# Performance work log

Measured on AMD Instinct MI355X. Metric: run time of the kernel, lower is better.

The kernel has to match this reference:

```python
import math
import jax, jax.numpy as jnp
import numpy as np
from jax.scipy.special import erf

D = 128                # cubic box / image size (even)
B, T = 4, 2            # particles, candidate poses per particle
GRID_DIST_DEGS = 8.0
GRID_STEP_DEGS = 2.0
PIXEL_SIZE = 1.5       # Angstrom / px
MAX_SHIFT_FRACTION = 0.2
TOP_K = 2
HALF_PARTICLE = 0.5 * D


def _rot_z(a):
    c, s = jnp.cos(a), jnp.sin(a)
    z, o = jnp.zeros_like(a), jnp.ones_like(a)
    return jnp.stack([jnp.stack([c, -s, z], -1),
                      jnp.stack([s, c, z], -1),
                      jnp.stack([z, z, o], -1)], -2)


def _rot_y(a):
    c, s = jnp.cos(a), jnp.sin(a)
    z, o = jnp.zeros_like(a), jnp.ones_like(a)
    return jnp.stack([jnp.stack([c, z, s], -1),
                      jnp.stack([z, o, z], -1),
                      jnp.stack([-s, z, c], -1)], -2)


def _euler_zyz_to_matrix(ang):
    # RELION convention ZYZ: R = Rz(a) @ Ry(b) @ Rz(c)
    return _rot_z(ang[..., 0]) @ _rot_y(ang[..., 1]) @ _rot_z(ang[..., 2])


def _so3_grid_rotmats():
    n = math.ceil(GRID_DIST_DEGS / GRID_STEP_DEGS)
    n = n if n % 2 == 1 else n + 1
    half = GRID_DIST_DEGS / 2.0
    a = np.linspace(-half, half, n)
    g = np.stack(np.meshgrid(a, a, a, indexing='ij'), -1).reshape(-1, 3)
    return _euler_zyz_to_matrix(jnp.deg2rad(jnp.asarray(g, jnp.float32)))


def _compute_dft(vol):
    # sinc^2 gridding pre-filter, then fftshifted rfftn of fftshifted volume
    d = vol.shape[-1]
    f = jnp.fft.fftshift(jnp.fft.fftfreq(d)).astype(vol.dtype)
    fz, fy, fx = jnp.meshgrid(f, f, f, indexing='ij')
    r = jnp.sqrt(fz * fz + fy * fy + fx * fx)
    vol = vol * jnp.sinc(r) ** 2
    dft = jnp.fft.rfftn(jnp.fft.fftshift(vol, axes=(-3, -2, -1)), axes=(-3, -2, -1))
    return jnp.fft.fftshift(dft, axes=(-3, -2))


def _trilinear_complex(vol, z, y, x):
    # trilinear interpolation into a complex 3D array, zero outside bounds
    Dz, Dy, Dx = vol.shape
    z0f, y0f, x0f = jnp.floor(z), jnp.floor(y), jnp.floor(x)
    fz, fy, fx = z - z0f, y - y0f, x - x0f
    z0, y0, x0 = z0f.astype(jnp.int32), y0f.astype(jnp.int32), x0f.astype(jnp.int32)

    def corner(zi, yi, xi, w):
        valid = (zi >= 0) & (zi < Dz) & (yi >= 0) & (yi < Dy) & (xi >= 0) & (xi < Dx)
        v = vol[jnp.clip(zi, 0, Dz - 1), jnp.clip(yi, 0, Dy - 1), jnp.clip(xi, 0, Dx - 1)]
        return jnp.where(valid, v * w, jnp.zeros((), vol.dtype))

    out = corner(z0, y0, x0, (1 - fz) * (1 - fy) * (1 - fx))
    out = out + corner(z0, y0, x0 + 1, (1 - fz) * (1 - fy) * fx)
    out = out + corner(z0, y0 + 1, x0, (1 - fz) * fy * (1 - fx))
    out = out + corner(z0, y0 + 1, x0 + 1, (1 - fz) * fy * fx)
    out = out + corner(z0 + 1, y0, x0, fz * (1 - fy) * (1 - fx))
    out = out + corner(z0 + 1, y0, x0 + 1, fz * (1 - fy) * fx)
    out = out + corner(z0 + 1, y0 + 1, x0, fz * fy * (1 - fx))
    out = out + corner(z0 + 1, y0 + 1, x0 + 1, fz * fy * fx)
    return out


def _extract_central_slices_rfft_3d(vol_rfft, d, rotmats):
    # rotated central-slice extraction from a fftshifted rfft 3D volume
    fy = jnp.fft.fftshift(jnp.fft.fftfreq(d)).astype(jnp.float32)
    fx = jnp.fft.rfftfreq(d).astype(jnp.float32)
    gy, gx = jnp.meshgrid(fy, fx, indexing='ij')            # (H, Wr)
    coords = jnp.stack([jnp.zeros_like(gy), gy, gx], -1)    # zyx, z=0 plane
    Rzyx = rotmats[..., ::-1, ::-1]                         # xyz rotmat -> zyx
    rot = jnp.einsum('...ij,hwj->...hwi', Rzyx, coords)     # (...,H,Wr,3)
    conj_mask = rot[..., 2] < 0                             # redundant half
    rot = jnp.where(conj_mask[..., None], -rot, rot)
    zi = rot[..., 0] * d + d // 2
    yi = rot[..., 1] * d + d // 2
    xi = rot[..., 2] * d
    s = _trilinear_complex(vol_rfft, zi, yi, xi)
    return jnp.where(conj_mask, jnp.conj(s), s)


def _forward(vol, imgs, ctf, rotmats, grid_rotmats):
    d = vol.shape[-1]
    vol_rfft = _compute_dft(vol)                            # (d, d, d//2+1)
    # _real_to_fourier
    fimg = jnp.fft.fftshift(
        jnp.fft.rfftn(jnp.fft.fftshift(imgs, axes=(-2, -1)), axes=(-2, -1)),
        axes=(-2,))                                         # (B, d, d//2+1)
    # compose pose candidates with the local SO3 grid: rotmats @ grid_rotmats
    exp_R = jnp.einsum('gjk,btij->btgik', grid_rotmats, rotmats)   # (B,T,G,3,3)
    projs = _extract_central_slices_rfft_3d(vol_rfft, d, exp_R)    # (B,T,G,H,Wr)
    projs = projs * ctf[:, None, None]
    # correlate_dft_2d
    prod = fimg[:, None, None] * jnp.conj(projs)
    prod = jnp.fft.ifftshift(prod, axes=(-2,))
    corrs = jnp.fft.ifftshift(jnp.fft.irfftn(prod, s=(d, d), axes=(-2, -1)),
                              axes=(-2, -1))                # (B,T,G,d,d) real
    # constrained peak search within max_shift_fraction window
    delta = math.ceil(d * (1.0 - MAX_SHIFT_FRACTION) / 2)
    h0 = delta
    c = corrs[..., h0:d - delta, h0:d - delta]
    maxJ = jnp.max(c, -1)
    argJ = jnp.argmax(c, -1)
    perImgCorr = jnp.max(maxJ, -1)                          # (B,T,G)
    argI = jnp.argmax(maxJ, -1)
    col = jnp.take_along_axis(argJ, argI[..., None], -1)[..., 0]
    shiftsXY = jnp.stack([h0 + col, h0 + argI], -1)         # (B,T,G,2) as (x,y)
    b = perImgCorr.shape[0]
    nrots = perImgCorr.shape[2]
    flat = perImgCorr.reshape(b, -1)                        # (B, T*G)
    maxCorrs, maxIdxs = jax.lax.top_k(flat, TOP_K)
    bestShifts = jnp.take_along_axis(shiftsXY.reshape(b, -1, 2),
                                     maxIdxs[..., None], axis=1)   # (B,K,2)
    mean = jnp.mean(flat, -1, keepdims=True)
    std = jnp.std(flat, -1, keepdims=True, ddof=1)
    comparedWeight = 0.5 * (1.0 + erf((maxCorrs - mean) / (std * 1.4142135623730951)))
    predShiftsAngs = -(bestShifts.astype(jnp.float32) - HALF_PARTICLE) * PIXEL_SIZE
    predRotMats = grid_rotmats[maxIdxs % nrots]             # (B,K,3,3)
    return maxCorrs, predRotMats, predShiftsAngs, comparedWeight


def setup_inputs() -> dict:
    key = jax.random.key(0)
    kv, ki, kc, kr = jax.random.split(key, 4)
    vol = jax.random.normal(kv, (D, D, D), jnp.float32)
    imgs = jax.random.normal(ki, (B, D, D), jnp.float32)
    ctf = jax.random.uniform(kc, (B, D, D // 2 + 1), jnp.float32, -1.0, 1.0)
    ang = jax.random.uniform(kr, (B, T, 3), jnp.float32, -np.pi, np.pi)
    rotmats = _euler_zyz_to_matrix(ang)
    grid_rotmats = _so3_grid_rotmats()
    return {"vol": vol, "imgs": imgs, "ctf": ctf, "rotmats": rotmats,
            "grid_rotmats": grid_rotmats}


def reference(vol, imgs, ctf, rotmats, grid_rotmats):
    return _forward(vol, imgs, ctf, rotmats, grid_rotmats)
```

## Files before the change

### kernel.cpp

```cpp
#include <hip/hip_runtime.h>
#include <hip/hip_fp16.h>
#include <math.h>
#include <float.h>

#define DD   128
#define KX   65
#define NB   4
#define NTT  2
#define NG   125
#define NBTG (NB*NTT*NG)
#define WIN  24
#define H0   52

#define QZ  132
#define QY  131
#define QX  68
#define QPLANE (QY*QX)
#define QN  (QZ*QY*QX)

typedef unsigned int u32;

__device__ __forceinline__ float2 cmul(float2 a, float2 b){
    return make_float2(a.x*b.x - a.y*b.y, a.x*b.y + a.y*b.x);
}

__device__ __forceinline__ void make_tw(float2* sTw, int tid){
    if (tid < 128){
        float s, c;
        sincosf((float)tid * (float)(M_PI/64.0), &s, &c);
        sTw[tid] = make_float2(c, s);
    }
}

__global__ __launch_bounds__(256) void k_stageA(const float* __restrict__ vol,
                       const float* __restrict__ imgs,
                       float2* __restrict__ A1, float2* __restrict__ B1,
                       uint4* __restrict__ Yz, int n4){
    __shared__ float2 sZ [16*DD];
    __shared__ float2 sZ2[16*DD];
    __shared__ float2 sTw[128];
    __shared__ float  sSinc[257];
    int tid = threadIdx.x;
    int bid = blockIdx.x;

    if (bid >= 642){
        int i = (bid - 642)*256 + tid;
        for (; i < n4; i += 256*256)
            Yz[i] = make_uint4(0,0,0,0);
        return;
    }
    make_tw(sTw, tid);

    if (bid < 512){
        for (int i = tid; i < 257; i += 256){
            float t = (float)i * (0.75f/256.f);
            float r = sqrtf(t);
            float s = (r > 0.f) ? (sinf((float)M_PI*r)/((float)M_PI*r)) : 1.f;
            sSinc[i] = s*s;
        }
        __syncthreads();
        int z = bid >> 2, q = bid & 3;
        int y0 = q*32;
        float fz = (z-64)*(1.0f/128.0f);
        float fz2 = fz*fz;
        for (int i = tid; i < 16*DD; i += 256){
            int p = i >> 7, x = i & 127;
            int yA = y0 + 2*p;
            float fx = (x-64)*(1.0f/128.0f);
            float fyA = (yA-64)*(1.0f/128.0f);
            float fyB = fyA + (1.0f/128.0f);
            float b2 = fz2 + fx*fx;
            float tA = (b2 + fyA*fyA) * (256.f/0.75f);
            float tB = (b2 + fyB*fyB) * (256.f/0.75f);
            int iA = min((int)tA, 255), iB = min((int)tB, 255);
            float frA = tA - (float)iA, frB = tB - (float)iB;
            float wA = sSinc[iA] + frA*(sSinc[iA+1]-sSinc[iA]);
            float wB = sSinc[iB] + frB*(sSinc[iB+1]-sSinc[iB]);
            float a = vol[(z*DD + yA)*DD + x] * wA;
            float b = vol[(z*DD + yA+1)*DD + x] * wB;
            sZ[i] = make_float2(a, b);
        }
        __syncthreads();
        for (int i = tid; i < 16*32; i += 256){
            int p = i >> 5, x1 = i & 31;
            int b0 = p*DD + x1;
            float2 a = sZ[b0], bb = sZ[b0+32], c2 = sZ[b0+64], d = sZ[b0+96];
            float acx=a.x+c2.x, acy=a.y+c2.y;
            float amx=a.x-c2.x, amy=a.y-c2.y;
            float bdx=bb.x+d.x, bdy=bb.y+d.y;
            float bmx=bb.x-d.x, bmy=bb.y-d.y;
            sZ[b0   ] = make_float2(acx+bdx, acy+bdy);
            sZ[b0+32] = make_float2(amx+bmy, amy-bmx);
            sZ[b0+64] = make_float2(acx-bdx, acy-bdy);
            sZ[b0+96] = make_float2(amx-bmy, amy+bmx);
        }
        __syncthreads();
        for (int i = tid; i < 16*32; i += 256){
            int p = i >> 5, r5 = i & 31;
            int c = r5 >> 3, x2 = r5 & 7;
            int b0 = p*DD + 32*c + x2;
            float2 u0 = sZ[b0], u1 = sZ[b0+8], u2 = sZ[b0+16], u3 = sZ[b0+24];
            float2 w1 = sTw[(8*c)&127];  w1.y = -w1.y;
            float2 w2 = sTw[(16*c)&127]; w2.y = -w2.y;
            float2 w3 = sTw[(24*c)&127]; w3.y = -w3.y;
            float2 t1 = cmul(u1,w1), t2 = cmul(u2,w2), t3 = cmul(u3,w3);
            float2 pp = make_float2(u0.x+t2.x, u0.y+t2.y);
            float2 qq = make_float2(u0.x-t2.x, u0.y-t2.y);
            float2 rr = make_float2(t1.x+t3.x, t1.y+t3.y);
            float2 ss = make_float2(t1.x-t3.x, t1.y-t3.y);
            sZ[b0   ] = make_float2(pp.x+rr.x, pp.y+rr.y);
            sZ[b0+8 ] = make_float2(qq.x+ss.y, qq.y-ss.x);
            sZ[b0+16] = make_float2(pp.x-rr.x, pp.y-rr.y);
            sZ[b0+24] = make_float2(qq.x-ss.y, qq.y+ss.x);
        }
        __syncthreads();
        for (int i = tid; i < 16*DD; i += 256){
            int p = i >> 7, k = i & 127;
            int c = k & 3, s = (k >> 2) & 3;
            const float2* v = &sZ[p*DD + 32*c + 8*s];
            float ar0=0,ai0=0,ar1=0,ai1=0;
            int j = 0;
            #pragma unroll
            for (int x2 = 0; x2 < 8; x2 += 2){
                float2 v0 = v[x2], v1 = v[x2+1];
                float2 e0 = sTw[j]; int jn = (j + k)&127;
                float2 e1 = sTw[jn];
                ar0 += v0.x*e0.x + v0.y*e0.y;  ai0 += v0.y*e0.x - v0.x*e0.y;
                ar1 += v1.x*e1.x + v1.y*e1.y;  ai1 += v1.y*e1.x - v1.x*e1.y;
                j = (jn + k)&127;
            }
            sZ2[i] = make_float2(ar0+ar1, ai0+ai1);
        }
        __syncthreads();
        for (int i = tid; i < 16*KX; i += 256){
            int p = i / KX, k = i - p*KX;
            float2 Zk = sZ2[p*DD + k];
            float2 Zm = sZ2[p*DD + ((128-k)&127)];
            float2 A = make_float2(0.5f*(Zk.x+Zm.x), 0.5f*(Zk.y-Zm.y));
            float Dx = Zk.x - Zm.x, Dy = Zk.y + Zm.y;
            float2 Bv = make_float2(0.5f*Dy, -0.5f*Dx);
            int yA = y0 + 2*p;
            A1[(z*DD + yA  )*KX + k] = A;
            A1[(z*DD + yA+1)*KX + k] = Bv;
        }
    } else {
        __syncthreads();
        int o = (bid - 512)*256 + tid;
        if (o >= NB*DD*KX) return;
        int b = o / (DD*KX);
        int r = o - b*DD*KX;
        int y = r / KX, k = r - y*KX;
        const float* row = imgs + (b*DD + y)*DD;
        float ar0=0,ai0=0,ar1=0,ai1=0,ar2=0,ai2=0,ar3=0,ai3=0;
        int i0=0, i1=k&127, i2=(2*k)&127, i3=(3*k)&127;
        int st = (4*k)&127;
        for (int x = 0; x < DD; x += 4){
            float v0=row[x], v1=row[x+1], v2=row[x+2], v3=row[x+3];
            float2 e0=sTw[i0], e1=sTw[i1], e2=sTw[i2], e3=sTw[i3];
            ar0 += v0*e0.x; ai0 -= v0*e0.y;
            ar1 += v1*e1.x; ai1 -= v1*e1.y;
            ar2 += v2*e2.x; ai2 -= v2*e2.y;
            ar3 += v3*e3.x; ai3 -= v3*e3.y;
            i0=(i0+st)&127; i1=(i1+st)&127; i2=(i2+st)&127; i3=(i3+st)&127;
        }
        B1[o] = make_float2(ar0+ar1+ar2+ar3, ai0+ai1+ai2+ai3);
    }
}

__global__ __launch_bounds__(256) void k_stageB(const float2* __restrict__ A1,
                       const float* __restrict__ ctf, const float2* __restrict__ B1,
                       float2* __restrict__ A2, float2* __restrict__ Fc){
    __shared__ float2 sU[32*KX];
    __shared__ float2 sTw[128];
    int tid = threadIdx.x;
    int bid = blockIdx.x;
    make_tw(sTw, tid);
    __syncthreads();

    if (bid < 512){
        int z = bid >> 2, c = bid & 3;
        const float2* base = A1 + z*DD*KX;
        for (int i = tid; i < 32*KX; i += 256){
            int n = i / KX, kk = i - n*KX;
            float2 a  = base[(n    )*KX + kk];
            float2 bb = base[(n+32)*KX + kk];
            float2 c2 = base[(n+64)*KX + kk];
            float2 d  = base[(n+96)*KX + kk];
            float acx = a.x + c2.x, acy = a.y + c2.y;
            float amx = a.x - c2.x, amy = a.y - c2.y;
            float bdx = bb.x + d.x, bdy = bb.y + d.y;
            float bmx = bb.x - d.x, bmy = bb.y - d.y;
            float2 u;
            if (c == 0)      u = make_float2(acx + bdx, acy + bdy);
            else if (c == 2) u = make_float2(acx - bdx, acy - bdy);
            else if (c == 1) u = make_float2(amx + bmy, amy - bmx);
            else             u = make_float2(amx - bmy, amy + bmx);
            sU[i] = u;
        }
        __syncthreads();
        float2 w1 = sTw[(8*c)&127];  w1.y = -w1.y;
        float2 w2 = sTw[(16*c)&127]; w2.y = -w2.y;
        float2 w3 = sTw[(24*c)&127]; w3.y = -w3.y;
        for (int i = tid; i < 8*KX; i += 256){
            int n2 = i / KX, kk = i - n2*KX;
            int b0 = n2*KX + kk;
            float2 u0 = sU[b0], u1 = sU[b0+8*KX], u2 = sU[b0+16*KX], u3 = sU[b0+24*KX];
            float2 t1 = cmul(u1,w1), t2 = cmul(u2,w2), t3 = cmul(u3,w3);
            float2 p = make_float2(u0.x+t2.x, u0.y+t2.y);
            float2 q = make_float2(u0.x-t2.x, u0.y-t2.y);
            float2 r = make_float2(t1.x+t3.x, t1.y+t3.y);
            float2 s = make_float2(t1.x-t3.x, t1.y-t3.y);
            sU[b0       ] = make_float2(p.x+r.x, p.y+r.y);
            sU[b0+ 8*KX ] = make_float2(q.x+s.y, q.y-s.x);
            sU[b0+16*KX ] = make_float2(p.x-r.x, p.y-r.y);
            sU[b0+24*KX ] = make_float2(q.x-s.y, q.y+s.x);
        }
        __syncthreads();
        for (int o = tid; o < 32*KX; o += 256){
            int m = o / KX, kk = o - m*KX;
            int ky = 4*m + c;
            int s4 = m & 3;
            const float2* v = &sU[(8*s4)*KX + kk];
            float ar0=0,ai0=0,ar1=0,ai1=0;
            int j = 0;
            #pragma unroll
            for (int n2 = 0; n2 < 8; n2 += 2){
                float2 v0 = v[n2*KX], v1 = v[(n2+1)*KX];
                float2 e0 = sTw[j]; int jn = (j + ky)&127;
                float2 e1 = sTw[jn];
                ar0 += v0.x*e0.x + v0.y*e0.y;  ai0 += v0.y*e0.x - v0.x*e0.y;
                ar1 += v1.x*e1.x + v1.y*e1.y;  ai1 += v1.y*e1.x - v1.x*e1.y;
                j = (jn + ky)&127;
            }
            A2[(z*DD + ky)*KX + kk] = make_float2(ar0+ar1, ai0+ai1);
        }
    } else {
        int o = (bid - 512)*256 + tid;
        if (o >= NB*DD*KX) return;
        int b = o / (DD*KX);
        int r = o - b*DD*KX;
        int h = r / KX, k = r - h*KX;
        int kky = (h + 64) & 127;
        const float2* col = B1 + b*DD*KX + k;
        float ar0=0,ai0=0,ar1=0,ai1=0,ar2=0,ai2=0,ar3=0,ai3=0;
        int i0=0, i1=kky&127, i2=(2*kky)&127, i3=(3*kky)&127;
        int st = (4*kky)&127;
        for (int y = 0; y < DD; y += 4){
            float2 v0=col[(y+0)*KX], v1=col[(y+1)*KX];
            float2 v2=col[(y+2)*KX], v3=col[(y+3)*KX];
            float2 e0=sTw[i0], e1=sTw[i1], e2=sTw[i2], e3=sTw[i3];
            ar0 += v0.x*e0.x + v0.y*e0.y;  ai0 += v0.y*e0.x - v0.x*e0.y;
            ar1 += v1.x*e1.x + v1.y*e1.y;  ai1 += v1.y*e1.x - v1.x*e1.y;
            ar2 += v2.x*e2.x + v2.y*e2.y;  ai2 += v2.y*e2.x - v2.x*e2.y;
            ar3 += v3.x*e3.x + v3.y*e3.y;  ai3 += v3.y*e3.x - v3.x*e3.y;
            i0=(i0+st)&127; i1=(i1+st)&127; i2=(i2+st)&127; i3=(i3+st)&127;
        }
        float sgn = ((h + k)&1) ? -1.f : 1.f;
        float cf = ctf[o];
        Fc[o] = make_float2((ar0+ar1+ar2+ar3)*sgn*cf, (ai0+ai1+ai2+ai3)*sgn*cf);
    }
}

__global__ __launch_bounds__(256) void k_volD(const float2* __restrict__ A2,
                       u32* __restrict__ Yh){
    __shared__ float2 sU[32*KX];
    __shared__ float2 sTw[128];
    int tid = threadIdx.x;
    int bid = blockIdx.x;
    int ky = bid >> 2, c = bid & 3;
    make_tw(sTw, tid);
    __syncthreads();

    const float2* base = A2 + ky*KX;
    for (int i = tid; i < 32*KX; i += 256){
        int n = i / KX, kk = i - n*KX;
        float2 a  = base[(n    )*DD*KX + kk];
        float2 bb = base[(n+32)*DD*KX + kk];
        float2 c2 = base[(n+64)*DD*KX + kk];
        float2 d  = base[(n+96)*DD*KX + kk];
        float acx = a.x + c2.x, acy = a.y + c2.y;
        float amx = a.x - c2.x, amy = a.y - c2.y;
        float bdx = bb.x + d.x, bdy = bb.y + d.y;
        float bmx = bb.x - d.x, bmy = bb.y - d.y;
        float2 u;
        if (c == 0)      u = make_float2(acx + bdx, acy + bdy);
        else if (c == 2) u = make_float2(acx - bdx, acy - bdy);
        else if (c == 1) u = make_float2(amx + bmy, amy - bmx);
        else             u = make_float2(amx - bmy, amy + bmx);
        sU[i] = u;
    }
    __syncthreads();
    float2 w1 = sTw[(8*c)&127];  w1.y = -w1.y;
    float2 w2 = sTw[(16*c)&127]; w2.y = -w2.y;
    float2 w3 = sTw[(24*c)&127]; w3.y = -w3.y;
    for (int i = tid; i < 8*KX; i += 256){
        int n2 = i / KX, kk = i - n2*KX;
        int b0 = n2*KX + kk;
        float2 u0 = sU[b0], u1 = sU[b0+8*KX], u2 = sU[b0+16*KX], u3 = sU[b0+24*KX];
        float2 t1 = cmul(u1,w1), t2 = cmul(u2,w2), t3 = cmul(u3,w3);
        float2 p = make_float2(u0.x+t2.x, u0.y+t2.y);
        float2 q = make_float2(u0.x-t2.x, u0.y-t2.y);
        float2 r = make_float2(t1.x+t3.x, t1.y+t3.y);
        float2 s = make_float2(t1.x-t3.x, t1.y-t3.y);
        sU[b0       ] = make_float2(p.x+r.x, p.y+r.y);
        sU[b0+ 8*KX ] = make_float2(q.x+s.y, q.y-s.x);
        sU[b0+16*KX ] = make_float2(p.x-r.x, p.y-r.y);
        sU[b0+24*KX ] = make_float2(q.x-s.y, q.y+s.x);
    }
    __syncthreads();
    int hy = (ky + 64) & 127;
    for (int o = tid; o < 32*KX; o += 256){
        int m = o / KX, kk = o - m*KX;
        int kz = 4*m + c;
        int hz = (kz + 64) & 127;
        int s4 = m & 3;
        const float2* v = &sU[(8*s4)*KX + kk];
        float ar0=0,ai0=0,ar1=0,ai1=0;
        int j = 0;
        #pragma unroll
        for (int n2 = 0; n2 < 8; n2 += 2){
            float2 v0 = v[n2*KX], v1 = v[(n2+1)*KX];
            float2 e0 = sTw[j]; int jn = (j + kz)&127;
            float2 e1 = sTw[jn];
            ar0 += v0.x*e0.x + v0.y*e0.y;  ai0 += v0.y*e0.x - v0.x*e0.y;
            ar1 += v1.x*e1.x + v1.y*e1.y;  ai1 += v1.y*e1.x - v1.x*e1.y;
            j = (jn + kz)&127;
        }
        float sgn = ((hz + hy + kk) & 1) ? -1.f : 1.f;
        __half2 hv = __floats2half2_rn((ar0+ar1)*sgn, (ai0+ai1)*sgn);
        u32 hp = *reinterpret_cast<u32*>(&hv);
        int z = hz + 1, y = hy + 1;
        Yh[2*((z*QY + y    )*QX + kk)    ] = hp;
        Yh[2*((z*QY + y - 1)*QX + kk) + 1] = hp;
    }
}

__device__ __forceinline__ float2 slice_point(const u32* __restrict__ Yh,
        float2 f, float xi, float zi, float yi){
    bool neg = xi < 0.f;
    if (neg){ xi = -xi; zi = 128.f - zi; yi = 128.f - yi; }
    xi = fminf(xi, 65.f);
    zi = fminf(fmaxf(zi, -1.f), 129.f);
    yi = fminf(fmaxf(yi, -1.f), 129.f);
    float zf = floorf(zi), yf = floorf(yi), xf = floorf(xi);
    float fz = zi - zf, fy = yi - yf, fx = xi - xf;
    int z0 = (int)zf, y0 = (int)yf, x0 = (int)xf;
    int qi = ((z0+1)*QY + (y0+1))*QX + x0;
    uint4 A = *reinterpret_cast<const uint4*>(Yh + 2*qi);
    uint4 B = *reinterpret_cast<const uint4*>(Yh + 2*(qi + QPLANE));
    float gx = 1.f - fx, gy = 1.f - fy, gz = 1.f - fz;
    float2 aL0 = __half22float2(*reinterpret_cast<const __half2*>(&A.x));
    float2 aH0 = __half22float2(*reinterpret_cast<const __half2*>(&A.y));
    float2 aL1 = __half22float2(*reinterpret_cast<const __half2*>(&A.z));
    float2 aH1 = __half22float2(*reinterpret_cast<const __half2*>(&A.w));
    float2 bL0 = __half22float2(*reinterpret_cast<const __half2*>(&B.x));
    float2 bH0 = __half22float2(*reinterpret_cast<const __half2*>(&B.y));
    float2 bL1 = __half22float2(*reinterpret_cast<const __half2*>(&B.z));
    float2 bH1 = __half22float2(*reinterpret_cast<const __half2*>(&B.w));
    float ar0 = aL0.x*gx + aL1.x*fx, ai0 = aL0.y*gx + aL1.y*fx;
    float ar1 = aH0.x*gx + aH1.x*fx, ai1 = aH0.y*gx + aH1.y*fx;
    float br0 = bL0.x*gx + bL1.x*fx, bi0 = bL0.y*gx + bL1.y*fx;
    float br1 = bH0.x*gx + bH1.x*fx, bi1 = bH0.y*gx + bH1.y*fx;
    float cr = ar0*gy + ar1*fy, ci = ai0*gy + ai1*fy;
    float dr = br0*gy + br1*fy, di = bi0*gy + bi1*fy;
    float sr = cr*gz + dr*fz,   si = ci*gz + di*fz;
    if (neg) si = -si;
    return make_float2(f.x*sr + f.y*si, f.y*sr - f.x*si);
}

__global__ __launch_bounds__(256,5) void k_main(
    const u32* __restrict__ Yh, const float2* __restrict__ Fc,
    const float* __restrict__ rotm, const float* __restrict__ grid,
    float* __restrict__ resVal, int2* __restrict__ resShift)
{
    __shared__ float2 sP[DD*16];
    __shared__ float2 sT[WIN*KX];
    __shared__ float2 sTw[128];
    __shared__ float  sM[9];
    __shared__ float  swv[4];
    __shared__ int    swi[4];

    int tid = threadIdx.x;
    int nb  = blockIdx.x;
    int blk = (nb & 7)*125 + (nb >> 3);
    int b  = blk / (NTT*NG);
    int rr = blk - b*NTT*NG;
    int t  = rr / NG;
    int g  = rr - t*NG;

    make_tw(sTw, tid);
    if (tid < 9){
        int i = tid/3, k = tid - 3*i;
        const float* R  = rotm + (b*NTT + t)*9;
        const float* Gm = grid + g*9;
        sM[tid] = R[i*3+0]*Gm[0*3+k] + R[i*3+1]*Gm[1*3+k] + R[i*3+2]*Gm[2*3+k];
    }
    __syncthreads();

    float M00=sM[0], M01=sM[1], M10=sM[3], M11=sM[4], M20=sM[6], M21=sM[7];
    const float2* FcB = Fc + b*DD*KX;

    if (tid < 128){
        int h = tid;
        float hf = (float)(h - 64);
        float xi = M01*hf + M00*64.f;
        float zi = M21*hf + M20*64.f + 64.f;
        float yi = M11*hf + M10*64.f + 64.f;
        sP[h] = slice_point(Yh, FcB[h*KX + 64], xi, zi, yi);
    }
    __syncthreads();
    if (tid < 96){
        int a = tid >> 2, p = tid & 3;
        int ry = (116 + a) & 127;
        int idx = (32*p*ry) & 127;
        float ar = 0.f, ai = 0.f;
        const float2* v = &sP[32*p];
        #pragma unroll 8
        for (int h2 = 0; h2 < 32; ++h2){
            float2 e = sTw[idx];
            float2 pv = v[h2];
            ar += pv.x*e.x - pv.y*e.y;
            ai += pv.x*e.y + pv.y*e.x;
            idx = (idx + ry) & 127;
        }
        sP[256 + tid] = make_float2(ar, ai);
    }
    __syncthreads();
    if (tid < 24){
        float2 p0 = sP[256 + tid*4 + 0];
        float2 p1 = sP[256 + tid*4 + 1];
        float2 p2 = sP[256 + tid*4 + 2];
        float2 p3 = sP[256 + tid*4 + 3];
        float sg = (tid & 1) ? -(1.f/128.f) : (1.f/128.f);
        sT[tid*KX + 64] = make_float2((p0.x+p1.x+p2.x+p3.x)*sg,
                                      (p0.y+p1.y+p2.y+p3.y)*sg);
    }
    __syncthreads();

    const int kk = tid & 15;
    const int h0 = tid >> 4;
    const float hf0 = (float)(h0 - 64);
    const float dxi = 16.f*M01, dzi = 16.f*M21, dyi = 16.f*M11;

    for (int cc = 0; cc < 4; ++cc){
        int w = cc*16 + kk;
        float wf = (float)w;
        float xi0 = M01*hf0 + M00*wf;
        float zi0 = M21*hf0 + M20*wf + 64.f;
        float yi0 = M11*hf0 + M10*wf + 64.f;
        int fidx = h0*KX + w;

        #pragma unroll 2
        for (int j = 0; j < 8; ++j){
            sP[tid + 256*j] = slice_point(Yh, FcB[fidx], xi0, zi0, yi0);
            xi0 += dxi; zi0 += dzi; yi0 += dyi; fidx += 16*KX;
        }
        __syncthreads();

        #pragma unroll
        for (int rep = 0; rep < 2; ++rep){
            int i = tid + 256*rep;
            float2 a  = sP[i];
            float2 bb = sP[i + 512];
            float2 c2 = sP[i + 1024];
            float2 d  = sP[i + 1536];
            float acx = a.x + c2.x, acy = a.y + c2.y;
            float amx = a.x - c2.x, amy = a.y - c2.y;
            float bdx = bb.x + d.x, bdy = bb.y + d.y;
            float bmx = bb.x - d.x, bmy = bb.y - d.y;
            sP[i       ] = make_float2(acx + bdx, acy + bdy);
            sP[i + 512 ] = make_float2(amx - bmy, amy + bmx);
            sP[i + 1024] = make_float2(acx - bdx, acy - bdy);
            sP[i + 1536] = make_float2(amx + bmy, amy - bmx);
        }
        __syncthreads();

        #pragma unroll
        for (int rep = 0; rep < 2; ++rep){
            int i = tid + 256*rep;
            int c = i >> 7, r7 = i & 127;
            int b0 = (c << 9) + r7;
            float2 u0 = sP[b0], u1 = sP[b0+128], u2 = sP[b0+256], u3 = sP[b0+384];
            float2 w1 = sTw[(8*c)&127], w2 = sTw[(16*c)&127], w3 = sTw[(24*c)&127];
            float2 t1 = cmul(u1,w1), t2 = cmul(u2,w2), t3 = cmul(u3,w3);
            float2 p  = make_float2(u0.x+t2.x, u0.y+t2.y);
            float2 qq = make_float2(u0.x-t2.x, u0.y-t2.y);
            float2 r  = make_float2(t1.x+t3.x, t1.y+t3.y);
            float2 s  = make_float2(t1.x-t3.x, t1.y-t3.y);
            sP[b0      ] = make_float2(p.x+r.x,  p.y+r.y);
            sP[b0 + 128] = make_float2(qq.x-s.y, qq.y+s.x);
            sP[b0 + 256] = make_float2(p.x-r.x,  p.y-r.y);
            sP[b0 + 384] = make_float2(qq.x+s.y, qq.y-s.x);
        }
        __syncthreads();

        for (int o = tid; o < 24*16; o += 256){
            int a = o >> 4, kx = o & 15;
            int ry = (116 + a) & 127;
            int c = ry & 3, s4 = (ry >> 2) & 3;
            const float2* v = &sP[(c << 9) + (s4 << 7) + kx];
            float ar0=0,ai0=0,ar1=0,ai1=0;
            int j2 = 0;
            #pragma unroll
            for (int n2 = 0; n2 < 8; n2 += 2){
                float2 v0 = v[n2*16], v1 = v[(n2+1)*16];
                float2 e0 = sTw[j2]; int jn = (j2 + ry)&127;
                float2 e1 = sTw[jn];
                ar0 += v0.x*e0.x - v0.y*e0.y;  ai0 += v0.x*e0.y + v0.y*e0.x;
                ar1 += v1.x*e1.x - v1.y*e1.y;  ai1 += v1.x*e1.y + v1.y*e1.x;
                j2 = (jn + ry)&127;
            }
            float sg = (a & 1) ? -(1.f/128.f) : (1.f/128.f);
            sT[a*KX + cc*16 + kx] = make_float2((ar0+ar1)*sg, (ai0+ai1)*sg);
        }
        __syncthreads();
    }

    float2* sPf = sP;
    for (int o = tid; o < WIN*31; o += 256){
        int a = o / 31, km1 = o - a*31;
        int k = km1 + 1;
        const float2* Trow = &sT[a*KX];
        float2 T1 = Trow[k], T2 = Trow[64-k];
        sPf[a*31 + km1]       = make_float2(T1.x + T2.x, T1.y - T2.y);
        sPf[744 + a*31 + km1] = make_float2(T1.x - T2.x, T1.y + T2.y);
    }
    __syncthreads();

    float* sC = reinterpret_cast<float*>(sP + 1488);
    for (int o = tid; o < WIN*WIN; o += 256){
        int a = o / WIN, bx = o - a*WIN;
        int rx = (116 + bx) & 127;
        const float2* Trow = &sT[a*KX];
        float2 T32 = Trow[32];
        float base = Trow[0].x + ((bx & 1) ? -Trow[64].x : Trow[64].x);
        int r4 = rx & 3;
        base += (r4==0) ?  2.f*T32.x : (r4==1) ? -2.f*T32.y
              : (r4==2) ? -2.f*T32.x :  2.f*T32.y;
        const float2* A = sPf + ((bx & 1) ? 744 : 0) + a*31 - 1;
        float acc0 = 0.f, acc1 = 0.f;
        int j1 = rx, j2 = (2*rx)&127;
        int st = (2*rx)&127;
        for (int k = 1; k < 31; k += 2){
            float2 e1 = sTw[j1]; float2 A1v = A[k];
            float2 e2 = sTw[j2]; float2 A2v = A[k+1];
            acc0 += A1v.x*e1.x - A1v.y*e1.y;
            acc1 += A2v.x*e2.x - A2v.y*e2.y;
            j1=(j1+st)&127; j2=(j2+st)&127;
        }
        {
            float2 e = sTw[(31*rx)&127]; float2 Av = A[31];
            acc0 += Av.x*e.x - Av.y*e.y;
        }
        sC[o] = (base + 2.f*(acc0+acc1))*(1.f/128.f);
    }
    __syncthreads();

    float best = -FLT_MAX; int bidx = 0x7fffffff;
    for (int i = tid; i < WIN*WIN; i += 256){
        float v = sC[i];
        if (v > best){ best = v; bidx = i; }
    }
    #pragma unroll
    for (int s = 32; s > 0; s >>= 1){
        float ov = __shfl_xor(best, s, 64);
        int   oi = __shfl_xor(bidx, s, 64);
        if (ov > best || (ov == best && oi < bidx)){ best = ov; bidx = oi; }
    }
    if ((tid & 63) == 0){ swv[tid>>6] = best; swi[tid>>6] = bidx; }
    __syncthreads();
    if (tid == 0){
        float bv = swv[0]; int bi = swi[0];
        #pragma unroll
        for (int w2 = 1; w2 < 4; ++w2){
            if (swv[w2] > bv || (swv[w2] == bv && swi[w2] < bi)){ bv = swv[w2]; bi = swi[w2]; }
        }
        int a = bi / WIN, bx = bi - a*WIN;
        resVal[blk] = bv;
        resShift[blk] = make_int2(H0 + bx, H0 + a);
    }
}

__global__ __launch_bounds__(256) void k_final(const float* __restrict__ resVal,
                        const int2* __restrict__ resShift,
                        const float* __restrict__ grid, float* __restrict__ out)
{
    __shared__ float sv[256];
    __shared__ int   si[256];
    __shared__ float sr[256];
    __shared__ float sMean;
    const int N = NTT*NG;
    int b = blockIdx.x, tid = threadIdx.x;
    const float* v = resVal + b*N;
    float myv = (tid < N) ? v[tid] : -FLT_MAX;

    sv[tid] = myv; si[tid] = (tid < N) ? tid : 0x7fffffff;
    __syncthreads();
    for (int s = 128; s > 0; s >>= 1){
        if (tid < s){
            float v2 = sv[tid+s]; int i2 = si[tid+s];
            if (v2 > sv[tid] || (v2 == sv[tid] && i2 < si[tid])){ sv[tid]=v2; si[tid]=i2; }
        }
        __syncthreads();
    }
    float v0 = sv[0]; int i0 = si[0];
    __syncthreads();

    bool act = (tid < N) && (tid != i0);
    sv[tid] = act ? myv : -FLT_MAX; si[tid] = act ? tid : 0x7fffffff;
    __syncthreads();
    for (int s = 128; s > 0; s >>= 1){
        if (tid < s){
            float v2 = sv[tid+s]; int i2 = si[tid+s];
            if (v2 > sv[tid] || (v2 == sv[tid] && i2 < si[tid])){ sv[tid]=v2; si[tid]=i2; }
        }
        __syncthreads();
    }
    float v1 = sv[0]; int i1 = si[0];
    __syncthreads();

    sr[tid] = (tid < N) ? myv : 0.f;
    __syncthreads();
    for (int s = 128; s > 0; s >>= 1){
        if (tid < s) sr[tid] += sr[tid+s];
        __syncthreads();
    }
    if (tid == 0) sMean = sr[0] / (float)N;
    __syncthreads();
    float mean = sMean;

    float d = (tid < N) ? (myv - mean) : 0.f;
    sr[tid] = d*d;
    __syncthreads();
    for (int s = 128; s > 0; s >>= 1){
        if (tid < s) sr[tid] += sr[tid+s];
        __syncthreads();
    }

    if (tid == 0){
        float stdv = sqrtf(sr[0] / (float)(N - 1));
        float vals[2] = {v0, v1};
        int   idxs[2] = {i0, i1};
        for (int k = 0; k < 2; ++k){
            out[b*2 + k] = vals[k];
            int gi = idxs[k] % NG;
            for (int j = 0; j < 9; ++j) out[8 + (b*2+k)*9 + j] = grid[gi*9 + j];
            int2 sh = resShift[b*N + idxs[k]];
            out[80 + (b*2+k)*2 + 0] = -((float)sh.x - 64.f)*1.5f;
            out[80 + (b*2+k)*2 + 1] = -((float)sh.y - 64.f)*1.5f;
            out[96 + b*2 + k] = 0.5f*(1.f + erff((vals[k] - mean)/(stdv*1.41421356237309515f)));
        }
    }
}

extern "C" void kernel_launch(void* const* d_in, const int* in_sizes, int n_in,
                              void* d_out, int out_size, void* d_ws, size_t ws_size,
                              hipStream_t stream)
{
    const float* vol  = (const float*)d_in[0];
    const float* imgs = (const float*)d_in[1];
    const float* ctf  = (const float*)d_in[2];
    const float* rotm = (const float*)d_in[3];
    const float* grid = (const float*)d_in[4];
    float* out = (float*)d_out;

    const size_t YH_BYTES  = (size_t)QN*8;
    const size_t A1_BYTES  = (size_t)DD*DD*KX*sizeof(float2);
    const size_t B1_BYTES  = (size_t)NB*DD*KX*sizeof(float2);

    char* ws = (char*)d_ws;
    u32*    Yh = (u32*)(ws);
    size_t off = YH_BYTES;
    float2* A1 = (float2*)(ws + off); off += A1_BYTES;
    float2* B1 = (float2*)(ws + off); off += B1_BYTES;
    float2* A2 = (float2*)(ws + off); off += A1_BYTES;
    float2* Fc = (float2*)(ws + off); off += B1_BYTES;
    float* resVal = (float*)(ws + off); off += (size_t)NBTG*sizeof(float);
    int2* resShift = (int2*)(ws + off); off += (size_t)NBTG*sizeof(int2);

    const int n4 = (int)(YH_BYTES / 16);
    k_stageA<<<898, 256, 0, stream>>>(vol, imgs, A1, B1, (uint4*)Yh, n4);
    k_stageB<<<642, 256, 0, stream>>>(A1, ctf, B1, A2, Fc);
    k_volD  <<<512, 256, 0, stream>>>(A2, Yh);
    k_main  <<<NBTG,256, 0, stream>>>(Yh, Fc, rotm, grid, resVal, resShift);
    k_final <<<NB,  256, 0, stream>>>(resVal, resShift, grid, out);
}
```

Baseline: 99.70 us.

## Fuse final top-k reduction into main kernel and interpolate in half2

Removes the separate k_final launch. The last k_main block to finish, found with an atomic counter that stage A resets, now runs the per-particle top-2 and mean/std reduction for all particles in a single block. Separately, slice_point's trilinear interpolation now runs in packed half2 FMAs instead of converting to float first. This cuts ALU and conversion work in the hot sampling path at the cost of reduced interpolation precision. The fused tail is serialized onto one block, which removes one launch but adds a short sequential tail.

```diff
diff --git a/kernel.cpp b/kernel.cpp
--- a/kernel.cpp
+++ b/kernel.cpp
@@ -35,7 +35,7 @@
 __global__ __launch_bounds__(256) void k_stageA(const float* __restrict__ vol,
                        const float* __restrict__ imgs,
                        float2* __restrict__ A1, float2* __restrict__ B1,
-                       uint4* __restrict__ Yz, int n4){
+                       uint4* __restrict__ Yz, int n4, int* __restrict__ cnt){
     __shared__ float2 sZ [16*DD];
     __shared__ float2 sZ2[16*DD];
     __shared__ float2 sTw[128];
@@ -44,6 +44,7 @@
     int bid = blockIdx.x;
 
     if (bid >= 642){
+        if (bid == 642 && tid == 0) *cnt = 0;
         int i = (bid - 642)*256 + tid;
         for (; i < n4; i += 256*256)
             Yz[i] = make_uint4(0,0,0,0);
@@ -344,26 +345,29 @@
     yi = fminf(fmaxf(yi, -1.f), 129.f);
     float zf = floorf(zi), yf = floorf(yi), xf = floorf(xi);
     float fz = zi - zf, fy = yi - yf, fx = xi - xf;
-    int z0 = (int)zf, y0 = (int)yf, x0 = (int)xf;
-    int qi = ((z0+1)*QY + (y0+1))*QX + x0;
+    int qi = (((int)zf + 1)*QY + ((int)yf + 1))*QX + (int)xf;
     uint4 A = *reinterpret_cast<const uint4*>(Yh + 2*qi);
     uint4 B = *reinterpret_cast<const uint4*>(Yh + 2*(qi + QPLANE));
-    float gx = 1.f - fx, gy = 1.f - fy, gz = 1.f - fz;
-    float2 aL0 = __half22float2(*reinterpret_cast<const __half2*>(&A.x));
-    float2 aH0 = __half22float2(*reinterpret_cast<const __half2*>(&A.y));
-    float2 aL1 = __half22float2(*reinterpret_cast<const __half2*>(&A.z));
-    float2 aH1 = __half22float2(*reinterpret_cast<const __half2*>(&A.w));
-    float2 bL0 = __half22float2(*reinterpret_cast<const __half2*>(&B.x));
-    float2 bH0 = __half22float2(*reinterpret_cast<const __half2*>(&B.y));
-    float2 bL1 = __half22float2(*reinterpret_cast<const __half2*>(&B.z));
-    float2 bH1 = __half22float2(*reinterpret_cast<const __half2*>(&B.w));
-    float ar0 = aL0.x*gx + aL1.x*fx, ai0 = aL0.y*gx + aL1.y*fx;
-    float ar1 = aH0.x*gx + aH1.x*fx, ai1 = aH0.y*gx + aH1.y*fx;
-    float br0 = bL0.x*gx + bL1.x*fx, bi0 = bL0.y*gx + bL1.y*fx;
-    float br1 = bH0.x*gx + bH1.x*fx, bi1 = bH0.y*gx + bH1.y*fx;
-    float cr = ar0*gy + ar1*fy, ci = ai0*gy + ai1*fy;
-    float dr = br0*gy + br1*fy, di = bi0*gy + bi1*fy;
-    float sr = cr*gz + dr*fz,   si = ci*gz + di*fz;
+    __half2 fxh = __float2half2_rn(fx);
+    __half2 fyh = __float2half2_rn(fy);
+    __half2 fzh = __float2half2_rn(fz);
+    __half2 aL0 = *reinterpret_cast<const __half2*>(&A.x);
+    __half2 aH0 = *reinterpret_cast<const __half2*>(&A.y);
+    __half2 aL1 = *reinterpret_cast<const __half2*>(&A.z);
+    __half2 aH1 = *reinterpret_cast<const __half2*>(&A.w);
+    __half2 bL0 = *reinterpret_cast<const __half2*>(&B.x);
+    __half2 bH0 = *reinterpret_cast<const __half2*>(&B.y);
+    __half2 bL1 = *reinterpret_cast<const __half2*>(&B.z);
+    __half2 bH1 = *reinterpret_cast<const __half2*>(&B.w);
+    __half2 a0 = __hfma2(fxh, __hsub2(aL1, aL0), aL0);
+    __half2 a1 = __hfma2(fxh, __hsub2(aH1, aH0), aH0);
+    __half2 b0 = __hfma2(fxh, __hsub2(bL1, bL0), bL0);
+    __half2 b1 = __hfma2(fxh, __hsub2(bH1, bH0), bH0);
+    __half2 c  = __hfma2(fyh, __hsub2(a1, a0), a0);
+    __half2 d  = __hfma2(fyh, __hsub2(b1, b0), b0);
+    __half2 s  = __hfma2(fzh, __hsub2(d, c), c);
+    float2 sv = __half22float2(s);
+    float sr = sv.x, si = sv.y;
     if (neg) si = -si;
     return make_float2(f.x*sr + f.y*si, f.y*sr - f.x*si);
 }
@@ -371,7 +375,8 @@
 __global__ __launch_bounds__(256,5) void k_main(
     const u32* __restrict__ Yh, const float2* __restrict__ Fc,
     const float* __restrict__ rotm, const float* __restrict__ grid,
-    float* __restrict__ resVal, int2* __restrict__ resShift)
+    float* __restrict__ resVal, int2* __restrict__ resShift,
+    float* __restrict__ out, int* __restrict__ cnt)
 {
     __shared__ float2 sP[DD*16];
     __shared__ float2 sT[WIN*KX];
@@ -379,6 +384,7 @@
     __shared__ float  sM[9];
     __shared__ float  swv[4];
     __shared__ int    swi[4];
+    __shared__ int    sLast;
 
     int tid = threadIdx.x;
     int nb  = blockIdx.x;
@@ -578,77 +584,79 @@
         int a = bi / WIN, bx = bi - a*WIN;
         resVal[blk] = bv;
         resShift[blk] = make_int2(H0 + bx, H0 + a);
-    }
-}
-
-__global__ __launch_bounds__(256) void k_final(const float* __restrict__ resVal,
-                        const int2* __restrict__ resShift,
-                        const float* __restrict__ grid, float* __restrict__ out)
-{
-    __shared__ float sv[256];
-    __shared__ int   si[256];
-    __shared__ float sr[256];
-    __shared__ float sMean;
-    const int N = NTT*NG;
-    int b = blockIdx.x, tid = threadIdx.x;
-    const float* v = resVal + b*N;
-    float myv = (tid < N) ? v[tid] : -FLT_MAX;
-
-    sv[tid] = myv; si[tid] = (tid < N) ? tid : 0x7fffffff;
-    __syncthreads();
-    for (int s = 128; s > 0; s >>= 1){
-        if (tid < s){
-            float v2 = sv[tid+s]; int i2 = si[tid+s];
-            if (v2 > sv[tid] || (v2 == sv[tid] && i2 < si[tid])){ sv[tid]=v2; si[tid]=i2; }
-        }
-        __syncthreads();
-    }
-    float v0 = sv[0]; int i0 = si[0];
-    __syncthreads();
-
-    bool act = (tid < N) && (tid != i0);
-    sv[tid] = act ? myv : -FLT_MAX; si[tid] = act ? tid : 0x7fffffff;
-    __syncthreads();
-    for (int s = 128; s > 0; s >>= 1){
-        if (tid < s){
-            float v2 = sv[tid+s]; int i2 = si[tid+s];
-            if (v2 > sv[tid] || (v2 == sv[tid] && i2 < si[tid])){ sv[tid]=v2; si[tid]=i2; }
-        }
-        __syncthreads();
-    }
-    float v1 = sv[0]; int i1 = si[0];
-    __syncthreads();
-
-    sr[tid] = (tid < N) ? myv : 0.f;
-    __syncthreads();
-    for (int s = 128; s > 0; s >>= 1){
-        if (tid < s) sr[tid] += sr[tid+s];
-        __syncthreads();
-    }
-    if (tid == 0) sMean = sr[0] / (float)N;
-    __syncthreads();
-    float mean = sMean;
-
-    float d = (tid < N) ? (myv - mean) : 0.f;
-    sr[tid] = d*d;
-    __syncthreads();
-    for (int s = 128; s > 0; s >>= 1){
-        if (tid < s) sr[tid] += sr[tid+s];
-        __syncthreads();
-    }
-
-    if (tid == 0){
-        float stdv = sqrtf(sr[0] / (float)(N - 1));
-        float vals[2] = {v0, v1};
-        int   idxs[2] = {i0, i1};
-        for (int k = 0; k < 2; ++k){
-            out[b*2 + k] = vals[k];
-            int gi = idxs[k] % NG;
-            for (int j = 0; j < 9; ++j) out[8 + (b*2+k)*9 + j] = grid[gi*9 + j];
-            int2 sh = resShift[b*N + idxs[k]];
-            out[80 + (b*2+k)*2 + 0] = -((float)sh.x - 64.f)*1.5f;
-            out[80 + (b*2+k)*2 + 1] = -((float)sh.y - 64.f)*1.5f;
-            out[96 + b*2 + k] = 0.5f*(1.f + erff((vals[k] - mean)/(stdv*1.41421356237309515f)));
+        __threadfence();
+        int prev = atomicAdd(cnt, 1);
+        sLast = (prev == NBTG - 1) ? 1 : 0;
+    }
+    __syncthreads();
+
+    if (sLast){
+        __threadfence();
+        float* sv   = reinterpret_cast<float*>(sP);
+        int*   sidx = reinterpret_cast<int*>(sP) + 256;
+        float* sr   = reinterpret_cast<float*>(sP) + 512;
+        const int N = NTT*NG;
+        for (int bb = 0; bb < NB; ++bb){
+            const float* v = resVal + bb*N;
+            float myv = (tid < N) ? v[tid] : -FLT_MAX;
+
+            sv[tid] = myv; sidx[tid] = (tid < N) ? tid : 0x7fffffff;
+            __syncthreads();
+            for (int s = 128; s > 0; s >>= 1){
+                if (tid < s){
+                    float v2 = sv[tid+s]; int i2 = sidx[tid+s];
+                    if (v2 > sv[tid] || (v2 == sv[tid] && i2 < sidx[tid])){ sv[tid]=v2; sidx[tid]=i2; }
+                }
+                __syncthreads();
+            }
+            float v0 = sv[0]; int i0 = sidx[0];
+            __syncthreads();
+
+            bool act = (tid < N) && (tid != i0);
+            sv[tid] = act ? myv : -FLT_MAX; sidx[tid] = act ? tid : 0x7fffffff;
+            __syncthreads();
+            for (int s = 128; s > 0; s >>= 1){
+                if (tid < s){
+                    float v2 = sv[tid+s]; int i2 = sidx[tid+s];
+                    if (v2 > sv[tid] || (v2 == sv[tid] && i2 < sidx[tid])){ sv[tid]=v2; sidx[tid]=i2; }
+                }
+                __syncthreads();
+            }
+            float v1 = sv[0]; int i1 = sidx[0];
+            __syncthreads();
+
+            sr[tid] = (tid < N) ? myv : 0.f;
+            __syncthreads();
+            for (int s = 128; s > 0; s >>= 1){
+                if (tid < s) sr[tid] += sr[tid+s];
+                __syncthreads();
+            }
+            float mean = sr[0] / (float)N;
+            __syncthreads();
+
+            float dd = (tid < N) ? (myv - mean) : 0.f;
+            sr[tid] = dd*dd;
+            __syncthreads();
+            for (int s = 128; s > 0; s >>= 1){
+                if (tid < s) sr[tid] += sr[tid+s];
+                __syncthreads();
+            }
+
+            if (tid == 0){
+                float stdv = sqrtf(sr[0] / (float)(N - 1));
+                float vals[2] = {v0, v1};
+                int   idxs[2] = {i0, i1};
+                for (int k2 = 0; k2 < 2; ++k2){
+                    out[bb*2 + k2] = vals[k2];
+                    int gi = idxs[k2] % NG;
+                    for (int j = 0; j < 9; ++j) out[8 + (bb*2+k2)*9 + j] = grid[gi*9 + j];
+                    int2 sh = resShift[bb*N + idxs[k2]];
+                    out[80 + (bb*2+k2)*2 + 0] = -((float)sh.x - 64.f)*1.5f;
+                    out[80 + (bb*2+k2)*2 + 1] = -((float)sh.y - 64.f)*1.5f;
+                    out[96 + bb*2 + k2] = 0.5f*(1.f + erff((vals[k2] - mean)/(stdv*1.41421356237309515f)));
+                }
+            }
+            __syncthreads();
         }
     }
 }
@@ -677,11 +685,11 @@
     float2* Fc = (float2*)(ws + off); off += B1_BYTES;
     float* resVal = (float*)(ws + off); off += (size_t)NBTG*sizeof(float);
     int2* resShift = (int2*)(ws + off); off += (size_t)NBTG*sizeof(int2);
+    int* cnt = (int*)(ws + off); off += sizeof(int);
 
     const int n4 = (int)(YH_BYTES / 16);
-    k_stageA<<<898, 256, 0, stream>>>(vol, imgs, A1, B1, (uint4*)Yh, n4);
+    k_stageA<<<898, 256, 0, stream>>>(vol, imgs, A1, B1, (uint4*)Yh, n4, cnt);
     k_stageB<<<642, 256, 0, stream>>>(A1, ctf, B1, A2, Fc);
     k_volD  <<<512, 256, 0, stream>>>(A2, Yh);
-    k_main  <<<NBTG,256, 0, stream>>>(Yh, Fc, rotm, grid, resVal, resShift);
-    k_final <<<NB,  256, 0, stream>>>(resVal, resShift, grid, out);
-}
+    k_main  <<<NBTG,256, 0, stream>>>(Yh, Fc, rotm, grid, resVal, resShift, out, cnt);
+}
```

New measurement: 134.0 us. +34.4%, slower.
